# Kernel tuning notes

Measured on AMD Instinct MI355X. Metric: run time of the kernel, lower is better.

The kernel has to match this reference:

```python
import jax, jax.numpy as jnp
import numpy as np

HEAD_SIZE = 128
EMB_SIZE = 2048


def setup_inputs() -> dict:
    key = jax.random.key(0)
    kx, kq, kk, kv = jax.random.split(key, 4)
    B, T, C = 4, 4096, EMB_SIZE
    scale = 1.0 / np.sqrt(C)
    x = jax.random.normal(kx, (B, T, C), dtype=jnp.float32)
    # Linear(emb, head, bias=False) weights stored as [emb, head] for x @ W
    Wq = jax.random.normal(kq, (C, HEAD_SIZE), dtype=jnp.float32) * scale
    Wk = jax.random.normal(kk, (C, HEAD_SIZE), dtype=jnp.float32) * scale
    Wv = jax.random.normal(kv, (C, HEAD_SIZE), dtype=jnp.float32) * scale
    return {"x": x, "Wq": Wq, "Wk": Wk, "Wv": Wv}


def reference(x, Wq, Wk, Wv):
    B, T, C = x.shape
    q = jnp.einsum("btc,ch->bth", x, Wq)
    k = jnp.einsum("btc,ch->bth", x, Wk)
    v = jnp.einsum("btc,ch->bth", x, Wv)
    # NOTE: original code scales by C ** (-0.05), where C = emb_size
    scale = jnp.asarray(C, dtype=x.dtype) ** (-0.05)
    wei = jnp.einsum("bqh,bkh->bqk", q, k) * scale  # [B, T, T]
    causal = jnp.tril(jnp.ones((T, T), dtype=bool))
    wei = jnp.where(causal[None, :, :], wei, -jnp.inf)
    wei = jax.nn.softmax(wei, axis=-1)
    # dropout(p=0.2) treated as identity (eval mode) for a deterministic reference
    out = jnp.einsum("bqk,bkh->bqh", wei, v)  # [B, T, head]
    return out
```

## Files before the change

### kernel.cpp

```cpp
#include <hip/hip_runtime.h>

#define LOG2E 1.4426950408889634f
#define SCALE 0.6830207f

typedef __attribute__((ext_vector_type(8))) _Float16 f16x8;
typedef __attribute__((ext_vector_type(4))) _Float16 f16x4;
typedef __attribute__((ext_vector_type(4))) float f32x4;

__device__ __forceinline__ void wg_barrier() {
  asm volatile("s_waitcnt lgkmcnt(0)\n\ts_barrier" ::: "memory");
}

__global__ __launch_bounds__(256) void prep_wf(const float* __restrict__ Wq,
    const float* __restrict__ Wk, const float* __restrict__ Wv,
    _Float16* __restrict__ Wf) {
  int t = blockIdx.x * 256 + threadIdx.x;
  int lane = t & 63;
  int nt = (t >> 6) % 24;
  int kc = t / (64 * 24);
  int g = lane >> 4, c = lane & 15;
  int n = nt * 16 + c;
  const float* W = (n < 128) ? Wq : ((n < 256) ? Wk : Wv);
  int nn = n & 127;
  f16x8 o;
#pragma unroll
  for (int j = 0; j < 8; ++j) {
    int k = kc * 32 + g * 8 + j;
    o[j] = (_Float16)W[k * 128 + nn];
  }
  *(f16x8*)(Wf + (size_t)t * 8) = o;
}

__global__ __launch_bounds__(256, 2) void proj(const float* __restrict__ x,
    const _Float16* __restrict__ Wf,
    _Float16* __restrict__ qo, _Float16* __restrict__ ko,
    _Float16* __restrict__ vTo) {
  __shared__ __align__(16) _Float16 As[2][32 * 72];
  int tid = threadIdx.x;
  int wave = tid >> 6, lane = tid & 63;
  int g = lane >> 4, c = lane & 15;
  int m0 = blockIdx.x * 32;
  int wn = wave * 6;
  const f32x4 fz = {0.f, 0.f, 0.f, 0.f};
  f32x4 acc[2][6];
#pragma unroll
  for (int a = 0; a < 2; ++a)
#pragma unroll
    for (int q = 0; q < 6; ++q) acc[a][q] = fz;

  int r = tid >> 3, c4 = tid & 7;
  const float* xp = x + (size_t)(m0 + r) * 2048 + c4 * 8;
  float4 pa[4], pb[4];
#pragma unroll
  for (int z = 0; z < 4; ++z) {
    pa[z] = *(const float4*)(xp + z * 64);
    pb[z] = *(const float4*)(xp + z * 64 + 4);
  }
  {
    f16x8 h8;
    h8[0] = (_Float16)pa[0].x; h8[1] = (_Float16)pa[0].y;
    h8[2] = (_Float16)pa[0].z; h8[3] = (_Float16)pa[0].w;
    h8[4] = (_Float16)pb[0].x; h8[5] = (_Float16)pb[0].y;
    h8[6] = (_Float16)pb[0].z; h8[7] = (_Float16)pb[0].w;
    *(f16x8*)(&As[0][0] + r * 72 + c4 * 8) = h8;
  }
  f16x8 bf[2][2][6];
#pragma unroll
  for (int kcl = 0; kcl < 2; ++kcl)
#pragma unroll
    for (int nt = 0; nt < 6; ++nt)
      bf[0][kcl][nt] = *(const f16x8*)(Wf +
          ((size_t)(kcl * 24 + wn + nt) * 64 + lane) * 8);
  wg_barrier();

#pragma unroll 4
  for (int kb = 0; kb < 32; ++kb) {
    if (kb + 1 < 32) {
#pragma unroll
      for (int kcl = 0; kcl < 2; ++kcl)
#pragma unroll
        for (int nt = 0; nt < 6; ++nt)
          bf[(kb + 1) & 1][kcl][nt] = *(const f16x8*)(Wf +
              ((size_t)(((kb + 1) * 2 + kcl) * 24 + wn + nt) * 64 + lane) * 8);
    }
    if (kb + 1 < 32) {
      int s = (kb + 1) & 3;
      f16x8 h8;
      h8[0] = (_Float16)pa[s].x; h8[1] = (_Float16)pa[s].y;
      h8[2] = (_Float16)pa[s].z; h8[3] = (_Float16)pa[s].w;
      h8[4] = (_Float16)pb[s].x; h8[5] = (_Float16)pb[s].y;
      h8[6] = (_Float16)pb[s].z; h8[7] = (_Float16)pb[s].w;
      *(f16x8*)(&As[(kb + 1) & 1][0] + r * 72 + c4 * 8) = h8;
    }
    if (kb + 4 < 32) {
      pa[kb & 3] = *(const float4*)(xp + (kb + 4) * 64);
      pb[kb & 3] = *(const float4*)(xp + (kb + 4) * 64 + 4);
    }
    const _Float16* Ab = &As[kb & 1][0];
#pragma unroll
    for (int kcl = 0; kcl < 2; ++kcl) {
      f16x8 af[2];
#pragma unroll
      for (int mt = 0; mt < 2; ++mt)
        af[mt] = *(const f16x8*)(Ab + (mt * 16 + c) * 72 + kcl * 32 + g * 8);
#pragma unroll
      for (int nt = 0; nt < 6; ++nt) {
#pragma unroll
        for (int mt = 0; mt < 2; ++mt)
          acc[mt][nt] = __builtin_amdgcn_mfma_f32_16x16x32_f16(
              af[mt], bf[kb & 1][kcl][nt], acc[mt][nt], 0, 0, 0);
      }
    }
    wg_barrier();
  }
#pragma unroll
  for (int mt = 0; mt < 2; ++mt) {
#pragma unroll
    for (int nt = 0; nt < 6; ++nt) {
      int n = (wn + nt) * 16 + c;
      int mat = n >> 7, col = n & 127;
#pragma unroll
      for (int i = 0; i < 4; ++i) {
        int row = m0 + mt * 16 + g * 4 + i;
        _Float16 hv = (_Float16)acc[mt][nt][i];
        if (mat == 0)      qo[(size_t)row * 128 + col] = hv;
        else if (mat == 1) ko[(size_t)row * 128 + col] = hv;
        else               vTo[(size_t)col * 16384 + row] = hv;
      }
    }
  }
}

__global__ __launch_bounds__(256, 3) void attn_part(
    const _Float16* __restrict__ qg, const _Float16* __restrict__ kg,
    const _Float16* __restrict__ vT,
    _Float16* __restrict__ Op, float* __restrict__ Ml) {
  __shared__ __align__(16) _Float16 Ks[64 * 136];
  __shared__ __align__(16) _Float16 Vt[128 * 72];
  __shared__ __align__(16) _Float16 Ps[4][16 * 72];
  int tid = threadIdx.x;
  int wave = tid >> 6, lane = tid & 63;
  int g = lane >> 4, c = lane & 15;
  int up = blockIdx.x;
  int xcd = up & 7, slot = up >> 3;
  int b = xcd >> 1;
  int t = (xcd & 1) * 144 + slot;
  int u = b * 288 + t;
  int k = 0, ob = 0;
  while (t >= ob + 8 * (k + 1)) { ob += 8 * (k + 1); ++k; }
  int qt = 8 * k + (t - ob) / (k + 1);
  int ch = (t - ob) % (k + 1);
  int q0 = qt * 64;
  int jbeg = ch * 8, jend = min(jbeg + 8, qt + 1);
  size_t base = (size_t)b * 4096 * 128;

  f16x8 qf[4];
#pragma unroll
  for (int kc = 0; kc < 4; ++kc)
    qf[kc] = *(const f16x8*)(qg + base + (size_t)(q0 + wave * 16 + c) * 128 + kc * 32 + g * 8);

  const f32x4 fz = {0.f, 0.f, 0.f, 0.f};
  f32x4 o[8];
#pragma unroll
  for (int hh = 0; hh < 8; ++hh) o[hh] = fz;
  float mrow = -1e30f, lrow = 0.f;

  int kr = tid >> 4, kc8 = tid & 15;
  int vh = tid >> 3, vt8 = tid & 7;
  uint4 rk[4], rv[4];
#pragma unroll
  for (int z = 0; z < 4; ++z) {
    rk[z] = *(const uint4*)(kg + base + (size_t)(jbeg * 64 + z * 16 + kr) * 128 + kc8 * 8);
    rv[z] = *(const uint4*)(vT + (size_t)(z * 32 + vh) * 16384 + b * 4096 + jbeg * 64 + vt8 * 8);
  }

  for (int j = jbeg; j < jend; ++j) {
    wg_barrier();
#pragma unroll
    for (int z = 0; z < 4; ++z) {
      *(uint4*)(Ks + (z * 16 + kr) * 136 + kc8 * 8) = rk[z];
      *(uint4*)(Vt + (z * 32 + vh) * 72 + vt8 * 8) = rv[z];
    }
    if (j + 1 < jend) {
#pragma unroll
      for (int z = 0; z < 4; ++z) {
        rk[z] = *(const uint4*)(kg + base + (size_t)((j + 1) * 64 + z * 16 + kr) * 128 + kc8 * 8);
        rv[z] = *(const uint4*)(vT + (size_t)(z * 32 + vh) * 16384 + b * 4096 + (j + 1) * 64 + vt8 * 8);
      }
    }
    wg_barrier();

    f32x4 s[4];
#pragma unroll
    for (int mt = 0; mt < 4; ++mt) s[mt] = fz;
#pragma unroll
    for (int kc = 0; kc < 4; ++kc) {
#pragma unroll
      for (int mt = 0; mt < 4; ++mt) {
        f16x8 kf = *(const f16x8*)(Ks + (mt * 16 + c) * 136 + kc * 32 + g * 8);
        s[mt] = __builtin_amdgcn_mfma_f32_16x16x32_f16(kf, qf[kc], s[mt], 0, 0, 0);
      }
    }
    bool diag = (j == qt);
    float tmax = -1e30f;
#pragma unroll
    for (int mt = 0; mt < 4; ++mt)
#pragma unroll
      for (int i = 0; i < 4; ++i) {
        float v = s[mt][i] * SCALE;
        if (diag && (mt * 16 + g * 4 + i) > (wave * 16 + c)) v = -1e30f;
        s[mt][i] = v;
        tmax = fmaxf(tmax, v);
      }
    tmax = fmaxf(tmax, __shfl_xor(tmax, 16, 64));
    tmax = fmaxf(tmax, __shfl_xor(tmax, 32, 64));
    float mnew = fmaxf(mrow, tmax);
    float alpha = __builtin_amdgcn_exp2f((mrow - mnew) * LOG2E);
    float rsum = 0.f;
#pragma unroll
    for (int mt = 0; mt < 4; ++mt)
#pragma unroll
      for (int i = 0; i < 4; ++i) {
        float e = __builtin_amdgcn_exp2f((s[mt][i] - mnew) * LOG2E);
        s[mt][i] = e;
        rsum += e;
      }
    rsum += __shfl_xor(rsum, 16, 64);
    rsum += __shfl_xor(rsum, 32, 64);
    lrow = lrow * alpha + rsum;
    mrow = mnew;
    int srcb = (lane & 48) + ((lane & 48) >> 2);
    float ar[4];
#pragma unroll
    for (int i = 0; i < 4; ++i) ar[i] = __shfl(alpha, srcb + i, 64);
#pragma unroll
    for (int hh = 0; hh < 8; ++hh)
#pragma unroll
      for (int i = 0; i < 4; ++i) o[hh][i] *= ar[i];
#pragma unroll
    for (int mt = 0; mt < 4; ++mt) {
      f16x4 pk;
#pragma unroll
      for (int i = 0; i < 4; ++i) pk[i] = (_Float16)s[mt][i];
      *(f16x4*)(&Ps[wave][0] + c * 72 + mt * 16 + g * 4) = pk;
    }
#pragma unroll
    for (int kc = 0; kc < 2; ++kc) {
      f16x8 pf = *(const f16x8*)(&Ps[wave][0] + c * 72 + kc * 32 + g * 8);
#pragma unroll
      for (int hh = 0; hh < 8; ++hh) {
        f16x8 vf = *(const f16x8*)(Vt + (hh * 16 + c) * 72 + kc * 32 + g * 8);
        o[hh] = __builtin_amdgcn_mfma_f32_16x16x32_f16(pf, vf, o[hh], 0, 0, 0);
      }
    }
  }
#pragma unroll
  for (int hh = 0; hh < 8; ++hh)
#pragma unroll
    for (int i = 0; i < 4; ++i) {
      int row = wave * 16 + g * 4 + i;
      Op[(size_t)u * 8192 + row * 128 + hh * 16 + c] = (_Float16)o[hh][i];
    }
  if (lane < 16) {
    int row = wave * 16 + lane;
    Ml[(size_t)u * 128 + row * 2]     = mrow;
    Ml[(size_t)u * 128 + row * 2 + 1] = lrow;
  }
}

__global__ __launch_bounds__(256) void attn_merge(const _Float16* __restrict__ Op,
    const float* __restrict__ Ml, float* __restrict__ out) {
  int up = blockIdx.x;
  int xcd = up & 7, slot = up >> 3;
  int b = xcd >> 1;
  int idx = (xcd & 1) * 128 + slot;
  int qt = idx >> 2, z = idx & 3;
  int k = qt >> 3;
  int nch = k + 1;
  int bb = 4 * k * (k + 1) + (qt & 7) * (k + 1);
  int u0 = b * 288 + bb;
  __shared__ float w[8][64];
  int tid = threadIdx.x;
  if (tid < 64) {
    float m[8], l[8];
    float M = -1e30f;
    for (int uu = 0; uu < nch; ++uu) {
      m[uu] = Ml[(size_t)(u0 + uu) * 128 + tid * 2];
      l[uu] = Ml[(size_t)(u0 + uu) * 128 + tid * 2 + 1];
      M = fmaxf(M, m[uu]);
    }
    float L = 0.f;
    for (int uu = 0; uu < nch; ++uu) {
      float e = __builtin_amdgcn_exp2f((m[uu] - M) * LOG2E);
      w[uu][tid] = e;
      L += l[uu] * e;
    }
    float iL = 1.0f / L;
    for (int uu = 0; uu < nch; ++uu) w[uu][tid] *= iL;
  }
  __syncthreads();
#pragma unroll
  for (int it = 0; it < 2; ++it) {
    int e0 = ((z * 2 + it) * 256 + tid) * 4;
    int row = e0 >> 7;
    const _Float16* opp = Op + (size_t)u0 * 8192 + e0;
    float ax = 0.f, ay = 0.f, az = 0.f, aw = 0.f;
    for (int uu = 0; uu < nch; ++uu) {
      f16x4 v = *(const f16x4*)(opp + (size_t)uu * 8192);
      float ww = w[uu][row];
      ax += ww * (float)v[0]; ay += ww * (float)v[1];
      az += ww * (float)v[2]; aw += ww * (float)v[3];
    }
    float4 r = {ax, ay, az, aw};
    *(float4*)(out + (size_t)b * 524288 + (size_t)qt * 8192 + e0) = r;
  }
}

extern "C" void kernel_launch(void* const* d_in, const int* in_sizes, int n_in,
                              void* d_out, int out_size, void* d_ws, size_t ws_size,
                              hipStream_t stream) {
  const float* x  = (const float*)d_in[0];
  const float* Wq = (const float*)d_in[1];
  const float* Wk = (const float*)d_in[2];
  const float* Wv = (const float*)d_in[3];
  const size_t NTOK = (size_t)16384 * 128;
  _Float16* q  = (_Float16*)d_ws;
  _Float16* k  = q + NTOK;
  _Float16* vT = k + NTOK;
  _Float16* Wf = vT + NTOK;
  _Float16* Op = Wf + (size_t)786432;
  float* Ml = (float*)(Op + (size_t)1152 * 8192);
  prep_wf<<<384, 256, 0, stream>>>(Wq, Wk, Wv, Wf);
  proj<<<512, 256, 0, stream>>>(x, Wf, q, k, vT);
  attn_part<<<1152, 256, 0, stream>>>(q, k, vT, Op, Ml);
  attn_merge<<<1024, 256, 0, stream>>>(Op, Ml, (float*)d_out);
}
```

Before: 328.7 us.

## Double-buffer K in LDS and load V fragments directly from global

New measurement: 358.8 us. 1.09x slower.

```diff
diff --git a/kernel.cpp b/kernel.cpp
--- a/kernel.cpp
+++ b/kernel.cpp
@@ -135,8 +135,7 @@
     const _Float16* __restrict__ qg, const _Float16* __restrict__ kg,
     const _Float16* __restrict__ vT,
     _Float16* __restrict__ Op, float* __restrict__ Ml) {
-  __shared__ __align__(16) _Float16 Ks[64 * 136];
-  __shared__ __align__(16) _Float16 Vt[128 * 72];
+  __shared__ __align__(16) _Float16 Ks[2][64 * 136];
   __shared__ __align__(16) _Float16 Ps[4][16 * 72];
   int tid = threadIdx.x;
   int wave = tid >> 6, lane = tid & 63;
@@ -153,6 +152,7 @@
   int q0 = qt * 64;
   int jbeg = ch * 8, jend = min(jbeg + 8, qt + 1);
   size_t base = (size_t)b * 4096 * 128;
+  const _Float16* vb = vT + (size_t)b * 4096;
 
   f16x8 qf[4];
 #pragma unroll
@@ -166,39 +166,49 @@
   float mrow = -1e30f, lrow = 0.f;
 
   int kr = tid >> 4, kc8 = tid & 15;
-  int vh = tid >> 3, vt8 = tid & 7;
-  uint4 rk[4], rv[4];
-#pragma unroll
-  for (int z = 0; z < 4; ++z) {
+  uint4 rk[4];
+#pragma unroll
+  for (int z = 0; z < 4; ++z)
     rk[z] = *(const uint4*)(kg + base + (size_t)(jbeg * 64 + z * 16 + kr) * 128 + kc8 * 8);
-    rv[z] = *(const uint4*)(vT + (size_t)(z * 32 + vh) * 16384 + b * 4096 + jbeg * 64 + vt8 * 8);
-  }
+#pragma unroll
+  for (int z = 0; z < 4; ++z)
+    *(uint4*)(&Ks[0][0] + (z * 16 + kr) * 136 + kc8 * 8) = rk[z];
+  if (jbeg + 1 < jend) {
+#pragma unroll
+    for (int z = 0; z < 4; ++z)
+      rk[z] = *(const uint4*)(kg + base + (size_t)((jbeg + 1) * 64 + z * 16 + kr) * 128 + kc8 * 8);
+  }
+  wg_barrier();
 
   for (int j = jbeg; j < jend; ++j) {
-    wg_barrier();
-#pragma unroll
-    for (int z = 0; z < 4; ++z) {
-      *(uint4*)(Ks + (z * 16 + kr) * 136 + kc8 * 8) = rk[z];
-      *(uint4*)(Vt + (z * 32 + vh) * 72 + vt8 * 8) = rv[z];
+    int p = (j - jbeg) & 1;
+    f16x8 vf[16];
+#pragma unroll
+    for (int hh = 0; hh < 8; ++hh)
+#pragma unroll
+      for (int kcl = 0; kcl < 2; ++kcl)
+        vf[hh * 2 + kcl] = *(const f16x8*)(vb +
+            (size_t)(hh * 16 + c) * 16384 + j * 64 + kcl * 32 + g * 8);
+
+    f32x4 s[4];
+#pragma unroll
+    for (int mt = 0; mt < 4; ++mt) s[mt] = fz;
+#pragma unroll
+    for (int kc = 0; kc < 4; ++kc) {
+#pragma unroll
+      for (int mt = 0; mt < 4; ++mt) {
+        f16x8 kf = *(const f16x8*)(&Ks[p][0] + (mt * 16 + c) * 136 + kc * 32 + g * 8);
+        s[mt] = __builtin_amdgcn_mfma_f32_16x16x32_f16(kf, qf[kc], s[mt], 0, 0, 0);
+      }
     }
     if (j + 1 < jend) {
 #pragma unroll
-      for (int z = 0; z < 4; ++z) {
-        rk[z] = *(const uint4*)(kg + base + (size_t)((j + 1) * 64 + z * 16 + kr) * 128 + kc8 * 8);
-        rv[z] = *(const uint4*)(vT + (size_t)(z * 32 + vh) * 16384 + b * 4096 + (j + 1) * 64 + vt8 * 8);
-      }
-    }
-    wg_barrier();
-
-    f32x4 s[4];
-#pragma unroll
-    for (int mt = 0; mt < 4; ++mt) s[mt] = fz;
-#pragma unroll
-    for (int kc = 0; kc < 4; ++kc) {
-#pragma unroll
-      for (int mt = 0; mt < 4; ++mt) {
-        f16x8 kf = *(const f16x8*)(Ks + (mt * 16 + c) * 136 + kc * 32 + g * 8);
-        s[mt] = __builtin_amdgcn_mfma_f32_16x16x32_f16(kf, qf[kc], s[mt], 0, 0, 0);
+      for (int z = 0; z < 4; ++z)
+        *(uint4*)(&Ks[p ^ 1][0] + (z * 16 + kr) * 136 + kc8 * 8) = rk[z];
+      if (j + 2 < jend) {
+#pragma unroll
+        for (int z = 0; z < 4; ++z)
+          rk[z] = *(const uint4*)(kg + base + (size_t)((j + 2) * 64 + z * 16 + kr) * 128 + kc8 * 8);
       }
     }
     bool diag = (j == qt);
@@ -248,11 +258,10 @@
     for (int kc = 0; kc < 2; ++kc) {
       f16x8 pf = *(const f16x8*)(&Ps[wave][0] + c * 72 + kc * 32 + g * 8);
 #pragma unroll
-      for (int hh = 0; hh < 8; ++hh) {
-        f16x8 vf = *(const f16x8*)(Vt + (hh * 16 + c) * 72 + kc * 32 + g * 8);
-        o[hh] = __builtin_amdgcn_mfma_f32_16x16x32_f16(pf, vf, o[hh], 0, 0, 0);
-      }
-    }
+      for (int hh = 0; hh < 8; ++hh)
+        o[hh] = __builtin_amdgcn_mfma_f32_16x16x32_f16(pf, vf[hh * 2 + kc], o[hh], 0, 0, 0);
+    }
+    wg_barrier();
   }
 #pragma unroll
   for (int hh = 0; hh < 8; ++hh)
```
